# Optimization experiments

Hardware: AMD Instinct MI355X
Metric: run time of the kernel (lower is better)

## Reference

```python
import jax, jax.numpy as jnp
import numpy as np

H = 1024  # hidden size

def _gru_seq(x_gates_tbg, h0, W_hh, b_hh):
    """x_gates_tbg: (T,B,3H) precomputed input-side gate activations (torch order r,z,n).
    h0: (B,H). Returns h_T (B,H)."""
    def step(h, xg):
        hg = h @ W_hh.T + b_hh                      # (B,3H)
        xr, xz, xn = jnp.split(xg, 3, axis=-1)
        hr, hz, hn = jnp.split(hg, 3, axis=-1)
        r = jax.nn.sigmoid(xr + hr)
        z = jax.nn.sigmoid(xz + hz)
        n = jnp.tanh(xn + r * hn)
        h_new = (1.0 - z) * n + z * h
        return h_new, None
    h_T, _ = jax.lax.scan(step, h0, x_gates_tbg)
    return h_T


def setup_inputs() -> dict:
    key = jax.random.key(0)
    ks = jax.random.split(key, 8)
    B, T, D_in, D_out = 64, 256, 1024, 1024
    s_in = 1.0 / np.sqrt(D_in)
    s_h = 1.0 / np.sqrt(H)
    return {
        "word_inputs": jax.random.normal(ks[0], (B, T, D_in), dtype=jnp.float32),
        "hidden": jnp.zeros((1, B, H), dtype=jnp.float32),
        "W_in": jax.random.normal(ks[1], (H, D_in), dtype=jnp.float32) * s_in,
        "b_in": jnp.zeros((H,), dtype=jnp.float32),
        "W_ih": jax.random.normal(ks[2], (3 * H, H), dtype=jnp.float32) * s_h,
        "b_ih": jnp.zeros((3 * H,), dtype=jnp.float32),
        "W_hh": jax.random.normal(ks[3], (3 * H, H), dtype=jnp.float32) * s_h,
        "b_hh": jnp.zeros((3 * H,), dtype=jnp.float32),
        "W_out": jax.random.normal(ks[4], (D_out, H), dtype=jnp.float32) * s_h,
        "b_out": jnp.zeros((D_out,), dtype=jnp.float32),
    }


def reference(word_inputs, hidden, W_in, b_in, W_ih, b_ih, W_hh, b_hh, W_out, b_out):
    # input linear: (B,T,D_in) -> (B,T,H)
    x = jnp.einsum('btd,hd->bth', word_inputs, W_in) + b_in
    # precompute input-side gate projections for all timesteps: (B,T,3H)
    x_gates = jnp.einsum('bth,gh->btg', x, W_ih) + b_ih
    x_gates_tbg = jnp.swapaxes(x_gates, 0, 1)       # (T,B,3H)
    h0 = hidden[0]                                   # single layer: (B,H)
    h_T = _gru_seq(x_gates_tbg, h0, W_hh, b_hh)      # (B,H)
    # output linear applied to last step only (equals out(output)[:, -1, :])
    out_last = h_T @ W_out.T + b_out                 # (B,out)
    hidden_out = h_T[None]                           # (1,B,H)
    return (out_last, hidden_out)
```

## Files before the change

### kernel.cpp

```cpp
#include <hip/hip_runtime.h>
#include <hip/hip_fp16.h>
#include <math.h>

#define HD 1024
#define BB 64
#define TT 256
#define GG (3 * HD)
#define NSCAN 64
#define NPROD 192

typedef _Float16 f16x8 __attribute__((ext_vector_type(8)));
typedef float f32x4 __attribute__((ext_vector_type(4)));

static constexpr size_t OFF_WCOMB = 0;
static constexpr size_t OFF_BCOMB = 12582912;
static constexpr size_t OFF_XG    = 12595200;
static constexpr size_t OFF_HTA   = 213921792;
static constexpr size_t OFF_HTB   = 214052864;
static constexpr size_t OFF_HFIN  = 214183936;
static constexpr size_t OFF_BAR   = 214446080;

__device__ __forceinline__ float sigmoidf_(float x) {
    return 1.0f / (1.0f + expf(-x));
}

__global__ void k_init(const float* __restrict__ hidden, __half* __restrict__ hta,
                       unsigned* __restrict__ bar) {
    int idx = blockIdx.x * 256 + threadIdx.x;
    hta[idx] = __float2half(hidden[idx]);
    if (idx < 17) bar[idx * 32] = 0u;
    if (idx < 256) bar[544 + idx] = 0u;
}

__global__ __launch_bounds__(256) void k_fold(const float* __restrict__ A,
                                              const float* __restrict__ Bw,
                                              float* __restrict__ C) {
    __shared__ __align__(16) float As[32][68];
    __shared__ __align__(16) float Bs[32][68];
    const int m0 = blockIdx.x * 64;
    const int n0 = blockIdx.y * 64;
    const int tid = threadIdx.x;
    const int r = (tid & 15) * 4;
    const int c = (tid >> 4) * 4;
    float acc[4][4] = {};
    for (int k0 = 0; k0 < HD; k0 += 32) {
        #pragma unroll
        for (int i = 0; i < 2; ++i) {
            int s = tid + i * 256;
            int row = s >> 3;
            int c4 = (s & 7) * 4;
            float4 v = *reinterpret_cast<const float4*>(&A[(size_t)(m0 + row) * HD + k0 + c4]);
            As[c4 + 0][row] = v.x; As[c4 + 1][row] = v.y;
            As[c4 + 2][row] = v.z; As[c4 + 3][row] = v.w;
        }
        #pragma unroll
        for (int i = 0; i < 2; ++i) {
            int s = tid + i * 256;
            int row = s >> 4;
            int c4 = (s & 15) * 4;
            float4 v = *reinterpret_cast<const float4*>(&Bw[(size_t)(k0 + row) * HD + n0 + c4]);
            *reinterpret_cast<float4*>(&Bs[row][c4]) = v;
        }
        __syncthreads();
        #pragma unroll
        for (int kk = 0; kk < 32; ++kk) {
            float4 av = *reinterpret_cast<const float4*>(&As[kk][r]);
            float4 bv = *reinterpret_cast<const float4*>(&Bs[kk][c]);
            float a_[4] = {av.x, av.y, av.z, av.w};
            float b_[4] = {bv.x, bv.y, bv.z, bv.w};
            #pragma unroll
            for (int i = 0; i < 4; ++i)
                #pragma unroll
                for (int j = 0; j < 4; ++j)
                    acc[i][j] += a_[i] * b_[j];
        }
        __syncthreads();
    }
    #pragma unroll
    for (int i = 0; i < 4; ++i) {
        float4 v = {acc[i][0], acc[i][1], acc[i][2], acc[i][3]};
        *reinterpret_cast<float4*>(&C[(size_t)(m0 + r + i) * HD + n0 + c]) = v;
    }
}

__global__ void k_bcomb(const float* __restrict__ W_ih, const float* __restrict__ b_in,
                        const float* __restrict__ b_ih, float* __restrict__ b_comb) {
    int g = (blockIdx.x * blockDim.x + threadIdx.x) >> 6;
    int lane = threadIdx.x & 63;
    float s = 0.f;
    for (int k = lane; k < HD; k += 64) s += W_ih[(size_t)g * HD + k] * b_in[k];
    #pragma unroll
    for (int off = 32; off > 0; off >>= 1) s += __shfl_down(s, off);
    if (lane == 0) b_comb[g] = s + b_ih[g];
}

__global__ __launch_bounds__(512, 2) void k_fused(
        const float* __restrict__ Whh, const float* __restrict__ bhh,
        const float* __restrict__ wi,  const float* __restrict__ Wc,
        const float* __restrict__ bc,  float* __restrict__ xg,
        const float* __restrict__ hidden,
        __half* __restrict__ hta, __half* __restrict__ htb,
        float* __restrict__ hfin, unsigned* __restrict__ bar) {
    __shared__ __align__(16) char lds[131072];
    const int tid = threadIdx.x;
    unsigned* const cnt = bar + 544;

    if (blockIdx.x < NSCAN) {
        char* const lh = lds;
        float* const cred = reinterpret_cast<float*>(lds);
        const int bid = blockIdx.x;
        const int j0 = bid * 16;
        const int w  = tid >> 6;
        const int l  = tid & 63;
        const int lg = l >> 4;
        const int ll = l & 15;
        const bool active = (w != 3 && w != 7);
        const int mt  = w & 3;
        const int ntA = (w < 4) ? 0 : 1;
        const int ntB = ntA + 2;
        const int fb = tid >> 4;
        const int fj = tid & 15;
        const int jg = j0 + fj;

        f16x8 areg[32];
        if (active) {
            const float* wrow = Whh + (size_t)(mt * HD + j0 + ll) * HD;
            #pragma unroll
            for (int kb = 0; kb < 32; ++kb) {
                int k0 = kb * 32 + lg * 8;
                float4 u0 = *reinterpret_cast<const float4*>(wrow + k0);
                float4 u1 = *reinterpret_cast<const float4*>(wrow + k0 + 4);
                f16x8 a;
                a[0] = (_Float16)u0.x; a[1] = (_Float16)u0.y;
                a[2] = (_Float16)u0.z; a[3] = (_Float16)u0.w;
                a[4] = (_Float16)u1.x; a[5] = (_Float16)u1.y;
                a[6] = (_Float16)u1.z; a[7] = (_Float16)u1.w;
                areg[kb] = a;
            }
        }
        const float br = bhh[jg], bz = bhh[HD + jg], bn = bhh[2 * HD + jg];
        float hold0 = hidden[(size_t)fb * HD + jg];
        float hold1 = hidden[(size_t)(fb + 32) * HD + jg];
        const int grp = bid >> 3;
        unsigned* const rootp = bar;
        unsigned* const grpp  = bar + 32 * (1 + grp);
        unsigned* const relp  = bar + 32 * (9 + grp);
        const int bA = ntA * 16 + ll, sA = bA & 7;
        const int bB = ntB * 16 + ll, sB = bB & 7;

        if (tid == 0) {
            while (__hip_atomic_load(&cnt[0], __ATOMIC_RELAXED, __HIP_MEMORY_SCOPE_AGENT) < 12u)
                __builtin_amdgcn_s_sleep(2);
            (void)__hip_atomic_load(&cnt[0], __ATOMIC_ACQUIRE, __HIP_MEMORY_SCOPE_AGENT);
        }
        __syncthreads();

        for (int t = 0; t < TT; ++t) {
            const __half* hc = (t & 1) ? htb : hta;
            __half* hnx = (t & 1) ? hta : htb;
            const size_t tb = (size_t)t * GG * BB;
            float xr0 = xg[tb + (size_t)jg * BB + fb];
            float xz0 = xg[tb + (size_t)(HD + jg) * BB + fb];
            float xn0 = xg[tb + (size_t)(2 * HD + jg) * BB + fb];
            float xr1 = xg[tb + (size_t)jg * BB + fb + 32];
            float xz1 = xg[tb + (size_t)(HD + jg) * BB + fb + 32];
            float xn1 = xg[tb + (size_t)(2 * HD + jg) * BB + fb + 32];
            #pragma unroll
            for (int i = 0; i < 16; ++i) {
                int c = tid + i * 512;
                int row = c >> 7, kc = c & 127;
                float4 v = *reinterpret_cast<const float4*>(
                    reinterpret_cast<const char*>(hc) + (size_t)row * 2048 + kc * 16);
                *reinterpret_cast<float4*>(lh + row * 2048 + ((kc ^ (row & 7)) << 4)) = v;
            }
            __syncthreads();
            f32x4 acc0 = {0.f, 0.f, 0.f, 0.f}, acc1 = {0.f, 0.f, 0.f, 0.f};
            if (active) {
                #pragma unroll
                for (int kb = 0; kb < 32; ++kb) {
                    int kc = kb * 4 + lg;
                    f16x8 b0 = *reinterpret_cast<const f16x8*>(lh + bA * 2048 + ((kc ^ sA) << 4));
                    f16x8 b1 = *reinterpret_cast<const f16x8*>(lh + bB * 2048 + ((kc ^ sB) << 4));
                    acc0 = __builtin_amdgcn_mfma_f32_16x16x32_f16(areg[kb], b0, acc0, 0, 0, 0);
                    acc1 = __builtin_amdgcn_mfma_f32_16x16x32_f16(areg[kb], b1, acc1, 0, 0, 0);
                }
            }
            __syncthreads();
            if (active) {
                int rb = mt * 16 + lg * 4;
                #pragma unroll
                for (int i = 0; i < 4; ++i) {
                    cred[(rb + i) * 68 + ntA * 16 + ll] = acc0[i];
                    cred[(rb + i) * 68 + ntB * 16 + ll] = acc1[i];
                }
            }
            __syncthreads();
            {
                float s0 = cred[fj * 68 + fb] + br;
                float s1 = cred[(16 + fj) * 68 + fb] + bz;
                float s2 = cred[(32 + fj) * 68 + fb] + bn;
                float rg = sigmoidf_(xr0 + s0);
                float zg = sigmoidf_(xz0 + s1);
                float ng = tanhf(xn0 + rg * s2);
                float hn0 = (1.0f - zg) * ng + zg * hold0;
                hold0 = hn0;
                hnx[(size_t)fb * HD + jg] = __float2half(hn0);
                float u0 = cred[fj * 68 + fb + 32] + br;
                float u1 = cred[(16 + fj) * 68 + fb + 32] + bz;
                float u2 = cred[(32 + fj) * 68 + fb + 32] + bn;
                float rg1 = sigmoidf_(xr1 + u0);
                float zg1 = sigmoidf_(xz1 + u1);
                float ng1 = tanhf(xn1 + rg1 * u2);
                float hn1 = (1.0f - zg1) * ng1 + zg1 * hold1;
                hold1 = hn1;
                hnx[(size_t)(fb + 32) * HD + jg] = __float2half(hn1);
                if (t == TT - 1) {
                    hfin[(size_t)jg * 64 + fb] = hn0;
                    hfin[(size_t)jg * 64 + fb + 32] = hn1;
                }
            }
            __syncthreads();
            if (tid == 0) {
                const unsigned e = (unsigned)(t + 1);
                unsigned old = __hip_atomic_fetch_add(grpp, 1u, __ATOMIC_ACQ_REL,
                                                      __HIP_MEMORY_SCOPE_AGENT);
                if (old == 8u * e - 1u) {
                    __hip_atomic_fetch_add(rootp, 1u, __ATOMIC_ACQ_REL,
                                           __HIP_MEMORY_SCOPE_AGENT);
                    while (__hip_atomic_load(rootp, __ATOMIC_RELAXED,
                                             __HIP_MEMORY_SCOPE_AGENT) < 8u * e)
                        __builtin_amdgcn_s_sleep(1);
                    (void)__hip_atomic_load(rootp, __ATOMIC_ACQUIRE, __HIP_MEMORY_SCOPE_AGENT);
                    __hip_atomic_store(relp, e, __ATOMIC_RELEASE, __HIP_MEMORY_SCOPE_AGENT);
                } else {
                    while (__hip_atomic_load(relp, __ATOMIC_RELAXED,
                                             __HIP_MEMORY_SCOPE_AGENT) < e)
                        __builtin_amdgcn_s_sleep(1);
                }
                (void)__hip_atomic_load(relp, __ATOMIC_ACQUIRE, __HIP_MEMORY_SCOPE_AGENT);
                if (t + 1 < TT) {
                    while (__hip_atomic_load(&cnt[t + 1], __ATOMIC_RELAXED,
                                             __HIP_MEMORY_SCOPE_AGENT) < 12u)
                        __builtin_amdgcn_s_sleep(1);
                    (void)__hip_atomic_load(&cnt[t + 1], __ATOMIC_ACQUIRE,
                                            __HIP_MEMORY_SCOPE_AGENT);
                }
            }
            __syncthreads();
        }
    } else {
        float* const As = reinterpret_cast<float*>(lds);
        float* const Bs = reinterpret_cast<float*>(lds + 9216);
        const int wid = blockIdx.x - NSCAN;
        const int r = (tid & 7) * 8;
        const int c = (tid >> 3) * 4;
        for (int item = wid; item < TT * 12; item += NPROD) {
            const int t  = item / 12;
            const int g0 = (item % 12) * 256;
            float acc[8][4] = {};
            for (int k0 = 0; k0 < HD; k0 += 32) {
                {
                    int s = tid;
                    int row = s >> 3, c4 = (s & 7) * 4;
                    float4 v = *reinterpret_cast<const float4*>(
                        &wi[((size_t)row * TT + t) * HD + k0 + c4]);
                    As[(c4 + 0) * 72 + row] = v.x; As[(c4 + 1) * 72 + row] = v.y;
                    As[(c4 + 2) * 72 + row] = v.z; As[(c4 + 3) * 72 + row] = v.w;
                }
                #pragma unroll
                for (int i = 0; i < 4; ++i) {
                    int s = tid + i * 512;
                    int row = s >> 3, c4 = (s & 7) * 4;
                    float4 v = *reinterpret_cast<const float4*>(
                        &Wc[(size_t)(g0 + row) * HD + k0 + c4]);
                    Bs[(c4 + 0) * 264 + row] = v.x; Bs[(c4 + 1) * 264 + row] = v.y;
                    Bs[(c4 + 2) * 264 + row] = v.z; Bs[(c4 + 3) * 264 + row] = v.w;
                }
                __syncthreads();
                #pragma unroll
                for (int kk = 0; kk < 32; ++kk) {
                    float4 a0 = *reinterpret_cast<const float4*>(&As[kk * 72 + r]);
                    float4 a1 = *reinterpret_cast<const float4*>(&As[kk * 72 + r + 4]);
                    float4 bv = *reinterpret_cast<const float4*>(&Bs[kk * 264 + c]);
                    float a_[8] = {a0.x, a0.y, a0.z, a0.w, a1.x, a1.y, a1.z, a1.w};
                    float b_[4] = {bv.x, bv.y, bv.z, bv.w};
                    #pragma unroll
                    for (int i = 0; i < 8; ++i)
                        #pragma unroll
                        for (int j = 0; j < 4; ++j)
                            acc[i][j] += a_[i] * b_[j];
                }
                __syncthreads();
            }
            const size_t base = (size_t)t * GG * BB;
            #pragma unroll
            for (int j = 0; j < 4; ++j) {
                int g = g0 + c + j;
                float bias = bc[g];
                float4 v0 = {acc[0][j] + bias, acc[1][j] + bias,
                             acc[2][j] + bias, acc[3][j] + bias};
                float4 v1 = {acc[4][j] + bias, acc[5][j] + bias,
                             acc[6][j] + bias, acc[7][j] + bias};
                *reinterpret_cast<float4*>(&xg[base + (size_t)g * BB + r]) = v0;
                *reinterpret_cast<float4*>(&xg[base + (size_t)g * BB + r + 4]) = v1;
            }
            __syncthreads();
            if (tid == 0)
                __hip_atomic_fetch_add(&cnt[t], 1u, __ATOMIC_RELEASE,
                                       __HIP_MEMORY_SCOPE_AGENT);
        }
    }
}

__global__ __launch_bounds__(256) void k_out(const float* __restrict__ ht,
                                             const float* __restrict__ Wout,
                                             const float* __restrict__ bout,
                                             float* __restrict__ out) {
    __shared__ __align__(16) float hs[128][68];
    __shared__ __align__(16) float wsl[16][128];
    const int tid = threadIdx.x;
    const int o0 = blockIdx.x * 16;
    const int b = tid & 63;
    const int obase = tid >> 6;
    float acc[4] = {};
    for (int k0 = 0; k0 < HD; k0 += 128) {
        #pragma unroll
        for (int i = 0; i < 8; ++i) {
            int s = tid + i * 256;
            int k = s >> 4;
            int bb = (s & 15) * 4;
            float4 v = *reinterpret_cast<const float4*>(&ht[(size_t)k0 * 64 + (size_t)s * 4]);
            *reinterpret_cast<float4*>(&hs[k][bb]) = v;
        }
        for (int s = tid; s < 16 * 32; s += 256) {
            int rr = s >> 5;
            int c4 = (s & 31) * 4;
            float4 v = *reinterpret_cast<const float4*>(&Wout[(size_t)(o0 + rr) * HD + k0 + c4]);
            *reinterpret_cast<float4*>(&wsl[rr][c4]) = v;
        }
        __syncthreads();
        for (int kk = 0; kk < 128; kk += 4) {
            float hv[4];
            #pragma unroll
            for (int u = 0; u < 4; ++u) hv[u] = hs[kk + u][b];
            #pragma unroll
            for (int i = 0; i < 4; ++i) {
                float4 wv = *reinterpret_cast<const float4*>(&wsl[obase + 4 * i][kk]);
                acc[i] += hv[0] * wv.x + hv[1] * wv.y + hv[2] * wv.z + hv[3] * wv.w;
            }
        }
        __syncthreads();
    }
    #pragma unroll
    for (int i = 0; i < 4; ++i) {
        int o = o0 + obase + 4 * i;
        out[(size_t)b * 1024 + o] = acc[i] + bout[o];
    }
}

__global__ void k_hout(const float* __restrict__ ht, float* __restrict__ outp) {
    int idx = blockIdx.x * 256 + threadIdx.x;
    int b = idx >> 10;
    int hh = idx & 1023;
    outp[idx] = ht[(size_t)hh * 64 + b];
}

extern "C" void kernel_launch(void* const* d_in, const int* in_sizes, int n_in,
                              void* d_out, int out_size, void* d_ws, size_t ws_size,
                              hipStream_t stream) {
    (void)in_sizes; (void)n_in; (void)out_size; (void)ws_size;
    const float* wi     = (const float*)d_in[0];
    const float* hidden = (const float*)d_in[1];
    const float* W_in   = (const float*)d_in[2];
    const float* b_in   = (const float*)d_in[3];
    const float* W_ih   = (const float*)d_in[4];
    const float* b_ih   = (const float*)d_in[5];
    const float* W_hh   = (const float*)d_in[6];
    const float* b_hh   = (const float*)d_in[7];
    const float* W_out  = (const float*)d_in[8];
    const float* b_out  = (const float*)d_in[9];

    char* ws = (char*)d_ws;
    float*    wcomb = (float*)(ws + OFF_WCOMB);
    float*    bcomb = (float*)(ws + OFF_BCOMB);
    float*    xg    = (float*)(ws + OFF_XG);
    __half*   hta   = (__half*)(ws + OFF_HTA);
    __half*   htb   = (__half*)(ws + OFF_HTB);
    float*    hfin  = (float*)(ws + OFF_HFIN);
    unsigned* bar   = (unsigned*)(ws + OFF_BAR);
    float*    out   = (float*)d_out;

    k_init<<<256, 256, 0, stream>>>(hidden, hta, bar);
    k_fold<<<dim3(48, 16), 256, 0, stream>>>(W_ih, W_in, wcomb);
    k_bcomb<<<768, 256, 0, stream>>>(W_ih, b_in, b_ih, bcomb);
    k_fused<<<256, 512, 0, stream>>>(W_hh, b_hh, wi, wcomb, bcomb, xg,
                                     hidden, hta, htb, hfin, bar);
    k_out<<<64, 256, 0, stream>>>(hfin, W_out, b_out, out);
    k_hout<<<256, 256, 0, stream>>>(hfin, out + 65536);
}
```

Baseline: 3.861 ms.

## Split h-state staging to overlap second-half load with first-half MFMA

The scan blocks now stage the h vector into LDS in two halves. The second half is fetched into registers while the MFMAs run on the first half, then written to LDS before the remaining MFMAs, which hides part of the global-load latency on the critical recurrence. The reduction buffer moves to a separate LDS region so it no longer aliases h, and the launch bound drops to one block per CU. The barrier also waits on producer readiness before arriving, drops the sleeps in its spin loops, and changes the padding in the producer GEMM's LDS tiles.

Measured after the change: 4.126 ms. 6.9% more time.

```diff
diff --git a/kernel.cpp b/kernel.cpp
--- a/kernel.cpp
+++ b/kernel.cpp
@@ -94,20 +94,20 @@
     if (lane == 0) b_comb[g] = s + b_ih[g];
 }
 
-__global__ __launch_bounds__(512, 2) void k_fused(
+__global__ __launch_bounds__(512, 1) void k_fused(
         const float* __restrict__ Whh, const float* __restrict__ bhh,
         const float* __restrict__ wi,  const float* __restrict__ Wc,
         const float* __restrict__ bc,  float* __restrict__ xg,
         const float* __restrict__ hidden,
         __half* __restrict__ hta, __half* __restrict__ htb,
         float* __restrict__ hfin, unsigned* __restrict__ bar) {
-    __shared__ __align__(16) char lds[131072];
+    __shared__ __align__(16) char lds[144128];
     const int tid = threadIdx.x;
     unsigned* const cnt = bar + 544;
 
     if (blockIdx.x < NSCAN) {
         char* const lh = lds;
-        float* const cred = reinterpret_cast<float*>(lds);
+        float* const cred = reinterpret_cast<float*>(lds + 131072);
         const int bid = blockIdx.x;
         const int j0 = bid * 16;
         const int w  = tid >> 6;
@@ -150,7 +150,7 @@
 
         if (tid == 0) {
             while (__hip_atomic_load(&cnt[0], __ATOMIC_RELAXED, __HIP_MEMORY_SCOPE_AGENT) < 12u)
-                __builtin_amdgcn_s_sleep(2);
+                __builtin_amdgcn_s_sleep(1);
             (void)__hip_atomic_load(&cnt[0], __ATOMIC_ACQUIRE, __HIP_MEMORY_SCOPE_AGENT);
         }
         __syncthreads();
@@ -165,19 +165,28 @@
             float xr1 = xg[tb + (size_t)jg * BB + fb + 32];
             float xz1 = xg[tb + (size_t)(HD + jg) * BB + fb + 32];
             float xn1 = xg[tb + (size_t)(2 * HD + jg) * BB + fb + 32];
-            #pragma unroll
-            for (int i = 0; i < 16; ++i) {
+            const char* hcB = reinterpret_cast<const char*>(hc);
+
+            #pragma unroll
+            for (int i = 0; i < 8; ++i) {
                 int c = tid + i * 512;
-                int row = c >> 7, kc = c & 127;
-                float4 v = *reinterpret_cast<const float4*>(
-                    reinterpret_cast<const char*>(hc) + (size_t)row * 2048 + kc * 16);
+                int row = c >> 6, kc = c & 63;
+                float4 v = *reinterpret_cast<const float4*>(hcB + (size_t)row * 2048 + kc * 16);
                 *reinterpret_cast<float4*>(lh + row * 2048 + ((kc ^ (row & 7)) << 4)) = v;
             }
             __syncthreads();
+
+            float4 pv[8];
+            #pragma unroll
+            for (int i = 0; i < 8; ++i) {
+                int c = tid + i * 512;
+                int row = c >> 6, kc = 64 + (c & 63);
+                pv[i] = *reinterpret_cast<const float4*>(hcB + (size_t)row * 2048 + kc * 16);
+            }
             f32x4 acc0 = {0.f, 0.f, 0.f, 0.f}, acc1 = {0.f, 0.f, 0.f, 0.f};
             if (active) {
                 #pragma unroll
-                for (int kb = 0; kb < 32; ++kb) {
+                for (int kb = 0; kb < 16; ++kb) {
                     int kc = kb * 4 + lg;
                     f16x8 b0 = *reinterpret_cast<const f16x8*>(lh + bA * 2048 + ((kc ^ sA) << 4));
                     f16x8 b1 = *reinterpret_cast<const f16x8*>(lh + bB * 2048 + ((kc ^ sB) << 4));
@@ -185,8 +194,22 @@
                     acc1 = __builtin_amdgcn_mfma_f32_16x16x32_f16(areg[kb], b1, acc1, 0, 0, 0);
                 }
             }
+            #pragma unroll
+            for (int i = 0; i < 8; ++i) {
+                int c = tid + i * 512;
+                int row = c >> 6, kc = 64 + (c & 63);
+                *reinterpret_cast<float4*>(lh + row * 2048 + ((kc ^ (row & 7)) << 4)) = pv[i];
+            }
             __syncthreads();
             if (active) {
+                #pragma unroll
+                for (int kb = 16; kb < 32; ++kb) {
+                    int kc = kb * 4 + lg;
+                    f16x8 b0 = *reinterpret_cast<const f16x8*>(lh + bA * 2048 + ((kc ^ sA) << 4));
+                    f16x8 b1 = *reinterpret_cast<const f16x8*>(lh + bB * 2048 + ((kc ^ sB) << 4));
+                    acc0 = __builtin_amdgcn_mfma_f32_16x16x32_f16(areg[kb], b0, acc0, 0, 0, 0);
+                    acc1 = __builtin_amdgcn_mfma_f32_16x16x32_f16(areg[kb], b1, acc1, 0, 0, 0);
+                }
                 int rb = mt * 16 + lg * 4;
                 #pragma unroll
                 for (int i = 0; i < 4; ++i) {
@@ -222,35 +245,33 @@
             __syncthreads();
             if (tid == 0) {
                 const unsigned e = (unsigned)(t + 1);
+                if (t + 1 < TT) {
+                    while (__hip_atomic_load(&cnt[t + 1], __ATOMIC_RELAXED,
+                                             __HIP_MEMORY_SCOPE_AGENT) < 12u)
+                        __builtin_amdgcn_s_sleep(1);
+                    (void)__hip_atomic_load(&cnt[t + 1], __ATOMIC_ACQUIRE,
+                                            __HIP_MEMORY_SCOPE_AGENT);
+                }
                 unsigned old = __hip_atomic_fetch_add(grpp, 1u, __ATOMIC_ACQ_REL,
                                                       __HIP_MEMORY_SCOPE_AGENT);
                 if (old == 8u * e - 1u) {
                     __hip_atomic_fetch_add(rootp, 1u, __ATOMIC_ACQ_REL,
                                            __HIP_MEMORY_SCOPE_AGENT);
                     while (__hip_atomic_load(rootp, __ATOMIC_RELAXED,
-                                             __HIP_MEMORY_SCOPE_AGENT) < 8u * e)
-                        __builtin_amdgcn_s_sleep(1);
+                                             __HIP_MEMORY_SCOPE_AGENT) < 8u * e) {}
                     (void)__hip_atomic_load(rootp, __ATOMIC_ACQUIRE, __HIP_MEMORY_SCOPE_AGENT);
                     __hip_atomic_store(relp, e, __ATOMIC_RELEASE, __HIP_MEMORY_SCOPE_AGENT);
                 } else {
                     while (__hip_atomic_load(relp, __ATOMIC_RELAXED,
-                                             __HIP_MEMORY_SCOPE_AGENT) < e)
-                        __builtin_amdgcn_s_sleep(1);
+                                             __HIP_MEMORY_SCOPE_AGENT) < e) {}
                 }
                 (void)__hip_atomic_load(relp, __ATOMIC_ACQUIRE, __HIP_MEMORY_SCOPE_AGENT);
-                if (t + 1 < TT) {
-                    while (__hip_atomic_load(&cnt[t + 1], __ATOMIC_RELAXED,
-                                             __HIP_MEMORY_SCOPE_AGENT) < 12u)
-                        __builtin_amdgcn_s_sleep(1);
-                    (void)__hip_atomic_load(&cnt[t + 1], __ATOMIC_ACQUIRE,
-                                            __HIP_MEMORY_SCOPE_AGENT);
-                }
             }
             __syncthreads();
         }
     } else {
         float* const As = reinterpret_cast<float*>(lds);
-        float* const Bs = reinterpret_cast<float*>(lds + 9216);
+        float* const Bs = reinterpret_cast<float*>(lds + 8704);
         const int wid = blockIdx.x - NSCAN;
         const int r = (tid & 7) * 8;
         const int c = (tid >> 3) * 4;
@@ -264,8 +285,8 @@
                     int row = s >> 3, c4 = (s & 7) * 4;
                     float4 v = *reinterpret_cast<const float4*>(
                         &wi[((size_t)row * TT + t) * HD + k0 + c4]);
-                    As[(c4 + 0) * 72 + row] = v.x; As[(c4 + 1) * 72 + row] = v.y;
-                    As[(c4 + 2) * 72 + row] = v.z; As[(c4 + 3) * 72 + row] = v.w;
+                    As[(c4 + 0) * 68 + row] = v.x; As[(c4 + 1) * 68 + row] = v.y;
+                    As[(c4 + 2) * 68 + row] = v.z; As[(c4 + 3) * 68 + row] = v.w;
                 }
                 #pragma unroll
                 for (int i = 0; i < 4; ++i) {
@@ -273,15 +294,15 @@
                     int row = s >> 3, c4 = (s & 7) * 4;
                     float4 v = *reinterpret_cast<const float4*>(
                         &Wc[(size_t)(g0 + row) * HD + k0 + c4]);
-                    Bs[(c4 + 0) * 264 + row] = v.x; Bs[(c4 + 1) * 264 + row] = v.y;
-                    Bs[(c4 + 2) * 264 + row] = v.z; Bs[(c4 + 3) * 264 + row] = v.w;
+                    Bs[(c4 + 0) * 260 + row] = v.x; Bs[(c4 + 1) * 260 + row] = v.y;
+                    Bs[(c4 + 2) * 260 + row] = v.z; Bs[(c4 + 3) * 260 + row] = v.w;
                 }
                 __syncthreads();
                 #pragma unroll
                 for (int kk = 0; kk < 32; ++kk) {
-                    float4 a0 = *reinterpret_cast<const float4*>(&As[kk * 72 + r]);
-                    float4 a1 = *reinterpret_cast<const float4*>(&As[kk * 72 + r + 4]);
-                    float4 bv = *reinterpret_cast<const float4*>(&Bs[kk * 264 + c]);
+                    float4 a0 = *reinterpret_cast<const float4*>(&As[kk * 68 + r]);
+                    float4 a1 = *reinterpret_cast<const float4*>(&As[kk * 68 + r + 4]);
+                    float4 bv = *reinterpret_cast<const float4*>(&Bs[kk * 260 + c]);
                     float a_[8] = {a0.x, a0.y, a0.z, a0.w, a1.x, a1.y, a1.z, a1.w};
                     float b_[4] = {bv.x, bv.y, bv.z, bv.w};
                     #pragma unroll
```
